# Kernel optimization log

Measured on AMD Instinct MI355X. Metric: run time of the kernel, lower is better.

Reference implementation:

```python
import jax, jax.numpy as jnp
import numpy as np

D_MODEL = 1024
N_HEADS = 16
HEAD_DIM = D_MODEL // N_HEADS


def setup_inputs() -> dict:
    key = jax.random.key(0)
    k1, k2, k3 = jax.random.split(key, 3)
    B, T = 4, 2048
    x = jax.random.normal(k1, (B, T, D_MODEL), dtype=jnp.float32)
    # torch Linear(d, 3d) weight is [3d, d]; y = x @ W^T. Store as [d, 3d] for x @ W.
    w_qkv = jax.random.normal(k2, (D_MODEL, 3 * D_MODEL), dtype=jnp.float32) * (D_MODEL ** -0.5)
    w_out = jax.random.normal(k3, (D_MODEL, D_MODEL), dtype=jnp.float32) * (D_MODEL ** -0.5)
    return {"x": x, "w_qkv": w_qkv, "w_out": w_out}


def reference(x, w_qkv, w_out):
    B, T, C = x.shape
    qkv = x @ w_qkv                             # [B, T, 3C]
    q, k, v = jnp.split(qkv, 3, axis=2)
    # [B, T, H, Dh] -> work in bthd layout via einsum
    q = q.reshape(B, T, N_HEADS, HEAD_DIM)
    k = k.reshape(B, T, N_HEADS, HEAD_DIM)
    v = v.reshape(B, T, N_HEADS, HEAD_DIM)
    scale = 1.0 / jnp.sqrt(jnp.asarray(HEAD_DIM, dtype=x.dtype))
    attn = jnp.einsum('bqhd,bkhd->bhqk', q, k) * scale   # [B, H, T, T]
    causal = jnp.tril(jnp.ones((T, T), dtype=bool))
    attn = jnp.where(causal, attn, jnp.asarray(-jnp.inf, dtype=attn.dtype))
    attn = jax.nn.softmax(attn, axis=-1)
    out = jnp.einsum('bhqk,bkhd->bqhd', attn, v).reshape(B, T, C)
    return out @ w_out
```

## Files before the change

kernel.cpp:

```cpp
#include <hip/hip_runtime.h>
#include <hip/hip_bf16.h>
#include <cstdint>


typedef __bf16 bf16x8 __attribute__((ext_vector_type(8)));
typedef __bf16 bf16x4 __attribute__((ext_vector_type(4)));
typedef float  f32x4  __attribute__((ext_vector_type(4)));
typedef float  f32x16 __attribute__((ext_vector_type(16)));
typedef unsigned int u32x4 __attribute__((ext_vector_type(4)));
typedef unsigned int u32x2 __attribute__((ext_vector_type(2)));

#define MFMA16(a, b, c) __builtin_amdgcn_mfma_f32_16x16x32_bf16((a), (b), (c), 0, 0, 0)
#define MFMA32(a, b, c) __builtin_amdgcn_mfma_f32_32x32x16_bf16((a), (b), (c), 0, 0, 0)

__device__ __forceinline__ float fexp2(float x) { return __builtin_amdgcn_exp2f(x); }

__device__ __forceinline__ void gload16(const void* g, void* lds) {
  __builtin_amdgcn_global_load_lds(
      (const __attribute__((address_space(1))) void*)(uintptr_t)g,
      (__attribute__((address_space(3))) void*)(uint32_t)(uintptr_t)lds,
      16, 0, 0);
}

__device__ __forceinline__ uint32_t cvtpk(float a, float b) {
  uint32_t r;
  asm("v_cvt_pk_bf16_f32 %0, %1, %2" : "=v"(r) : "v"(a), "v"(b));
  return r;
}

__device__ __forceinline__ float halfswap(float x, int hi) {
  uint32_t u = __builtin_bit_cast(uint32_t, x);
  u32x2 rr = __builtin_amdgcn_permlane32_swap(u, u, false, false);
  return __builtin_bit_cast(float, hi ? rr.x : rr.y);
}

__global__ __launch_bounds__(256) void k_f32_to_bf16(const float* __restrict__ in,
                                                     __bf16* __restrict__ out, int n) {
  int idx = (blockIdx.x * 256 + threadIdx.x) * 4;
  int stride = gridDim.x * 256 * 4;
  for (; idx < n; idx += stride) {
    float4 v = *(const float4*)(in + idx);
    bf16x4 o = { (__bf16)v.x, (__bf16)v.y, (__bf16)v.z, (__bf16)v.w };
    *(bf16x4*)(out + idx) = o;
  }
}

__global__ __launch_bounds__(256) void k_transpose_f32_bf16(const float* __restrict__ in,
                                                            __bf16* __restrict__ out,
                                                            int R, int C, float scale, int nscale) {
  __shared__ float t[64][65];
  const int r0 = blockIdx.y * 64, c0 = blockIdx.x * 64;
  const int tx = threadIdx.x & 15, ty = threadIdx.x >> 4;
#pragma unroll
  for (int rr = 0; rr < 4; ++rr) {
    int r = ty + rr * 16;
    float4 v = *(const float4*)(in + (size_t)(r0 + r) * C + c0 + tx * 4);
    t[r][tx * 4 + 0] = v.x; t[r][tx * 4 + 1] = v.y;
    t[r][tx * 4 + 2] = v.z; t[r][tx * 4 + 3] = v.w;
  }
  __syncthreads();
#pragma unroll
  for (int rr = 0; rr < 4; ++rr) {
    int c = ty + rr * 16;
    float sc = (c0 + c < nscale) ? scale : 1.0f;
    bf16x4 o = { (__bf16)(t[tx * 4 + 0][c] * sc), (__bf16)(t[tx * 4 + 1][c] * sc),
                 (__bf16)(t[tx * 4 + 2][c] * sc), (__bf16)(t[tx * 4 + 3][c] * sc) };
    *(bf16x4*)(out + (size_t)(c0 + c) * R + r0 + tx * 4) = o;
  }
}

template <typename OutT>
__global__ __launch_bounds__(256) void k_gemm_bt(const __bf16* __restrict__ A,
                                                 const __bf16* __restrict__ BT,
                                                 OutT* __restrict__ C,
                                                 int M, int N, int K) {
  __shared__ __align__(16) __bf16 At[128 * 32];
  __shared__ __align__(16) __bf16 Bt[128 * 32];
  const int tid = threadIdx.x;
  const int l = tid & 63, w = tid >> 6;
  const int wr = w >> 1, wc = w & 1;
  const int lr = l & 15, lk = l >> 4;
  const int bm0 = blockIdx.y * 128, bn0 = blockIdx.x * 128;

  const int sm = w * 16 + (l >> 2);
  const int sk = ((l & 3) ^ ((l >> 3) & 3)) * 8;
  const int xko = (lk ^ ((lr >> 1) & 3)) * 8;
  const __bf16* ga0 = A + (size_t)(bm0 + sm) * K + sk;
  const __bf16* ga1 = A + (size_t)(bm0 + 64 + sm) * K + sk;
  const __bf16* gb0 = BT + (size_t)(bn0 + sm) * K + sk;
  const __bf16* gb1 = BT + (size_t)(bn0 + 64 + sm) * K + sk;
  char* lA = (char*)At + w * 1024;
  char* lB = (char*)Bt + w * 1024;

  const f32x4 fz = {0.f, 0.f, 0.f, 0.f};
  f32x4 acc[4][4];
#pragma unroll
  for (int i = 0; i < 4; ++i) {
#pragma unroll
    for (int j = 0; j < 4; ++j) acc[i][j] = fz;
  }

  for (int k0 = 0; k0 < K; k0 += 32) {
    gload16(ga0, lA);
    gload16(ga1, lA + 4096);
    gload16(gb0, lB);
    gload16(gb1, lB + 4096);
    ga0 += 32; ga1 += 32; gb0 += 32; gb1 += 32;
    __syncthreads();
    bf16x8 af[4], bfr[4];
#pragma unroll
    for (int i = 0; i < 4; ++i)
      af[i] = *(const bf16x8*)(At + (wr * 64 + i * 16 + lr) * 32 + xko);
#pragma unroll
    for (int j = 0; j < 4; ++j)
      bfr[j] = *(const bf16x8*)(Bt + (wc * 64 + j * 16 + lr) * 32 + xko);
#pragma unroll
    for (int i = 0; i < 4; ++i) {
#pragma unroll
      for (int j = 0; j < 4; ++j) acc[i][j] = MFMA16(af[i], bfr[j], acc[i][j]);
    }
    __syncthreads();
  }

#pragma unroll
  for (int i = 0; i < 4; ++i) {
#pragma unroll
    for (int j = 0; j < 4; ++j) {
#pragma unroll
      for (int jj = 0; jj < 4; ++jj) {
        int row = bm0 + wr * 64 + i * 16 + lk * 4 + jj;
        int col = bn0 + wc * 64 + j * 16 + lr;
        C[(size_t)row * N + col] = (OutT)acc[i][j][jj];
      }
    }
  }
}

__global__ __launch_bounds__(512, 2) void k_gemm256(const __bf16* __restrict__ A,
                                                    const __bf16* __restrict__ BT,
                                                    __bf16* __restrict__ C,
                                                    __bf16* __restrict__ VT,
                                                    int M, int N, int K) {
  __shared__ __align__(16) __bf16 SMEM[4][2][128 * 64];
  __bf16 (*Als)[2][128 * 64] = &SMEM[0];
  __bf16 (*Bls)[2][128 * 64] = &SMEM[2];
  const int tid = threadIdx.x;
  const int l = tid & 63, w = tid >> 6;
  const int wm = w >> 2, wn = w & 3;
  const int wnh = wn >> 1, wnl = wn & 1;
  const int lr = l & 15, lk = l >> 4, lr7 = lr & 7;
  const int bm0 = blockIdx.y * 256, bn0 = blockIdx.x * 256;
  const int sr0 = w * 8 + (l >> 3);
  const int sc0 = ((l & 7) ^ (l >> 3)) * 8;
  const int xo0 = (lk ^ lr7) * 8;
  const int xo1 = ((4 + lk) ^ lr7) * 8;

#define STAGE_A(KT, H) do {                                                      \
    const __bf16* s_ = A + (size_t)(bm0 + (H) * 128 + sr0) * K + (KT) * 64 + sc0; \
    char* d_ = (char*)&Als[(KT) & 1][H][0] + w * 1024;                            \
    gload16(s_, d_);                                                              \
    gload16(s_ + (size_t)64 * K, d_ + 8192);                                      \
  } while (0)
#define STAGE_B(KT, H) do {                                                       \
    const __bf16* s_ = BT + (size_t)(bn0 + (H) * 128 + sr0) * K + (KT) * 64 + sc0; \
    char* d_ = (char*)&Bls[(KT) & 1][H][0] + w * 1024;                             \
    gload16(s_, d_);                                                               \
    gload16(s_ + (size_t)64 * K, d_ + 8192);                                       \
  } while (0)
#define LDA(SLOT, QM) do {                                                  \
    _Pragma("unroll") for (int f_ = 0; f_ < 4; ++f_) {                      \
      const __bf16* rp_ = &Als[SLOT][wm][0] + ((QM) * 64 + f_ * 16 + lr) * 64; \
      af[f_][0] = *(const bf16x8*)(rp_ + xo0);                              \
      af[f_][1] = *(const bf16x8*)(rp_ + xo1);                              \
    }                                                                       \
  } while (0)
#define LDB(SLOT, QN) do {                                                  \
    _Pragma("unroll") for (int g_ = 0; g_ < 2; ++g_) {                      \
      const __bf16* rp_ = &Bls[SLOT][wnh][0] + (wnl * 64 + (QN) * 32 + g_ * 16 + lr) * 64; \
      bq[QN][g_][0] = *(const bf16x8*)(rp_ + xo0);                          \
      bq[QN][g_][1] = *(const bf16x8*)(rp_ + xo1);                          \
    }                                                                       \
  } while (0)
#define MFMAQ(QM, QN) do {                                                  \
    __builtin_amdgcn_s_setprio(1);                                          \
    _Pragma("unroll") for (int f_ = 0; f_ < 4; ++f_) {                      \
      _Pragma("unroll") for (int g_ = 0; g_ < 2; ++g_) {                    \
        acc[(QM) * 4 + f_][(QN) * 2 + g_] =                                 \
            MFMA16(af[f_][0], bq[QN][g_][0], acc[(QM) * 4 + f_][(QN) * 2 + g_]); \
        acc[(QM) * 4 + f_][(QN) * 2 + g_] =                                 \
            MFMA16(af[f_][1], bq[QN][g_][1], acc[(QM) * 4 + f_][(QN) * 2 + g_]); \
      }                                                                     \
    }                                                                       \
    __builtin_amdgcn_s_setprio(0);                                          \
  } while (0)
#define BAR() asm volatile("s_barrier" ::: "memory")
#define VMCNT2() asm volatile("s_waitcnt vmcnt(2)" ::: "memory")
#define VMCNT0() asm volatile("s_waitcnt vmcnt(0)" ::: "memory")

  f32x4 acc[8][4];
  const f32x4 fz = {0.f, 0.f, 0.f, 0.f};
#pragma unroll
  for (int m = 0; m < 8; ++m) {
#pragma unroll
    for (int n = 0; n < 4; ++n) acc[m][n] = fz;
  }
  bf16x8 af[4][2], bq[2][2][2];

  STAGE_A(0, 0); STAGE_A(0, 1); STAGE_B(0, 0); STAGE_B(0, 1); STAGE_A(1, 0);
  VMCNT2();
  BAR();

  const int NT = K >> 7;
#pragma unroll 1
  for (int t = 0; t < NT; ++t) {
    const int k1 = 2 * t + 1, k2 = 2 * t + 2, k3 = 2 * t + 3;
    const bool last = (t == NT - 1);
    LDA(0, 0); LDB(0, 0);
    STAGE_A(k1, 1);
    BAR(); MFMAQ(0, 0); BAR();
    LDB(0, 1);
    STAGE_B(k1, 0);
    BAR(); MFMAQ(0, 1); BAR();
    LDA(0, 1);
    STAGE_B(k1, 1);
    BAR(); MFMAQ(1, 1); BAR();
    if (!last) { STAGE_A(k2, 0); VMCNT2(); } else { VMCNT0(); }
    BAR(); MFMAQ(1, 0); BAR();
    LDA(1, 0); LDB(1, 0);
    if (!last) STAGE_A(k2, 1);
    BAR(); MFMAQ(0, 0); BAR();
    LDB(1, 1);
    if (!last) STAGE_B(k2, 0);
    BAR(); MFMAQ(0, 1); BAR();
    LDA(1, 1);
    if (!last) STAGE_B(k2, 1);
    BAR(); MFMAQ(1, 1); BAR();
    if (!last) { STAGE_A(k3, 0); VMCNT2(); }
    BAR(); MFMAQ(1, 0); BAR();
  }

  if (VT != nullptr && bn0 >= 2048) {
    __bf16* tb = &SMEM[0][0][0];
    const int LDT = 264;
    const int bb = bm0 >> 11, tbase = bm0 & 2047;
#pragma unroll 1
    for (int hp = 0; hp < 2; ++hp) {
      if (wnh == hp) {
#pragma unroll
        for (int m = 0; m < 8; ++m) {
          const int tt = wm * 128 + (m >> 2) * 64 + (m & 3) * 16 + lk * 4;
#pragma unroll
          for (int n = 0; n < 4; ++n) {
            const int lcol = wnl * 64 + (n >> 1) * 32 + (n & 1) * 16 + lr;
            bf16x4 o = { (__bf16)acc[m][n][0], (__bf16)acc[m][n][1],
                         (__bf16)acc[m][n][2], (__bf16)acc[m][n][3] };
            *(bf16x4*)(tb + lcol * LDT + tt) = o;
          }
        }
      }
      __syncthreads();
#pragma unroll
      for (int it = 0; it < 8; ++it) {
        const int slot = it * 512 + tid;
        const int r = slot >> 5, toff = (slot & 31) * 8;
        bf16x8 v = *(const bf16x8*)(tb + r * LDT + toff);
        const int vcol = (bn0 - 2048) + hp * 128 + r;
        const int hc = vcol >> 6, d = vcol & 63;
        *(bf16x8*)(VT + ((size_t)((bb * 16 + hc) * 64 + d)) * 2048 + tbase + toff) = v;
      }
      if (hp == 0) __syncthreads();
    }
  } else {
#pragma unroll
    for (int m = 0; m < 8; ++m) {
      const int row = bm0 + wm * 128 + (m >> 2) * 64 + (m & 3) * 16 + lk * 4;
#pragma unroll
      for (int n = 0; n < 4; ++n) {
        const int col = bn0 + wn * 64 + (n >> 1) * 32 + (n & 1) * 16 + lr;
#pragma unroll
        for (int jj = 0; jj < 4; ++jj)
          C[(size_t)(row + jj) * N + col] = (__bf16)acc[m][n][jj];
      }
    }
  }
#undef STAGE_A
#undef STAGE_B
#undef LDA
#undef LDB
#undef MFMAQ
#undef BAR
#undef VMCNT2
#undef VMCNT0
}

__global__ __launch_bounds__(256, 2) void k_attn(const __bf16* __restrict__ qkv,
                                                 const __bf16* __restrict__ vt,
                                                 __bf16* __restrict__ ctx) {
  const int id = blockIdx.x;
  const int wg = (id & 7) * 64 + (id >> 3);
  const int p  = wg & 7;
  const int hb = wg >> 3;
  const int h = hb & 15, b = hb >> 4;

  const int l = threadIdx.x & 63, w = threadIdx.x >> 6;
  const int q = l & 31, hi = l >> 5, l7 = l & 7;

  __shared__ __align__(16) __bf16 KVs[3][2][64 * 64];

  const int srow = w * 8 + (l >> 3);
  const int scol = ((l & 7) ^ (l >> 3)) * 8;

  const __bf16* gK0 = qkv + (size_t)(b * 2048 + srow) * 3072 + 1024 + h * 64 + scol;
  const __bf16* gV0 = vt + ((size_t)((b * 16 + h) * 64 + srow)) * 2048 + scol;

  const float NEG = -1e30f;

  bf16x8 ones;
#pragma unroll
  for (int i = 0; i < 8; ++i) ones[i] = (__bf16)1.0f;

#define STG(BUF) do {                                                        \
    char* dK_ = (char*)&KVs[BUF][0][0] + w * 1024;                           \
    char* dV_ = (char*)&KVs[BUF][1][0] + w * 1024;                           \
    gload16(kp, dK_);                                                        \
    gload16(kp + (size_t)32 * 3072, dK_ + 4096);                             \
    gload16(vp, dV_);                                                        \
    gload16(vp + (size_t)32 * 2048, dV_ + 4096);                             \
    kp += (size_t)64 * 3072;                                                 \
    vp += 64;                                                                \
  } while (0)

#define ATTN_TILE(BUF, NXT) do {                                             \
    const int kv0 = kvt * 64;                                                \
    if (kvt + 1 < nkv) {                                                     \
      STG(NXT);                                                              \
      asm volatile("s_waitcnt vmcnt(4)" ::: "memory");                       \
    } else {                                                                 \
      asm volatile("s_waitcnt vmcnt(0)" ::: "memory");                       \
    }                                                                        \
    asm volatile("s_barrier" ::: "memory");                                  \
    if (kvt <= kvlast) {                                                     \
      const __bf16* Kb = &KVs[BUF][0][0];                                    \
      const __bf16* Vb = &KVs[BUF][1][0];                                    \
      f32x16 s0 = (f32x16)(0.0f), s1 = (f32x16)(0.0f);                       \
      __builtin_amdgcn_s_setprio(1);                                         \
      _Pragma("unroll") for (int d0 = 0; d0 < 4; ++d0) {                     \
        bf16x8 k0 = *(const bf16x8*)(Kb + (size_t)q * 64 + (((d0 * 2 + hi) ^ l7) * 8)); \
        bf16x8 k1 = *(const bf16x8*)(Kb + (size_t)(32 + q) * 64 + (((d0 * 2 + hi) ^ l7) * 8)); \
        s0 = MFMA32(k0, qf[d0], s0);                                         \
        s1 = MFMA32(k1, qf[d0], s1);                                         \
      }                                                                      \
      __builtin_amdgcn_s_setprio(0);                                         \
      if (kvt == kvlast) {                                                   \
        _Pragma("unroll") for (int r = 0; r < 16; ++r) {                     \
          const int kl = (r & 3) + 8 * (r >> 2) + 4 * hi;                    \
          if (kv0 + kl > qg) s0[r] = NEG;                                    \
          if (kv0 + 32 + kl > qg) s1[r] = NEG;                               \
        }                                                                    \
      }                                                                      \
      float t[8];                                                            \
      _Pragma("unroll") for (int i = 0; i < 8; ++i)                          \
        t[i] = fmaxf(fmaxf(s0[i], s0[i + 8]), fmaxf(s1[i], s1[i + 8]));      \
      _Pragma("unroll") for (int i = 0; i < 4; ++i) t[i] = fmaxf(t[i], t[i + 4]); \
      float mt = fmaxf(fmaxf(t[0], t[1]), fmaxf(t[2], t[3]));                \
      mt = fmaxf(mt, halfswap(mt, hi));                                      \
      if (!__all(mt - m_run <= 8.0f)) {                                      \
        const float al = fexp2(m_run - mt);                                  \
        _Pragma("unroll") for (int r = 0; r < 16; ++r) {                     \
          o0[r] *= al; o1[r] *= al; os[r] *= al;                             \
        }                                                                    \
        m_run = mt;                                                          \
      }                                                                      \
      _Pragma("unroll") for (int r = 0; r < 16; ++r) {                       \
        s0[r] = fexp2(s0[r] - m_run);                                        \
        s1[r] = fexp2(s1[r] - m_run);                                        \
      }                                                                      \
      uint32_t c0[8], c1[8];                                                 \
      _Pragma("unroll") for (int j = 0; j < 8; ++j) {                        \
        c0[j] = cvtpk(s0[2 * j], s0[2 * j + 1]);                             \
        c1[j] = cvtpk(s1[2 * j], s1[2 * j + 1]);                             \
      }                                                                      \
      u32x4 pk[4];                                                           \
      {                                                                      \
        u32x2 r0 = __builtin_amdgcn_permlane32_swap(c0[0], c0[2], false, false); \
        u32x2 r1 = __builtin_amdgcn_permlane32_swap(c0[1], c0[3], false, false); \
        u32x2 r2 = __builtin_amdgcn_permlane32_swap(c0[4], c0[6], false, false); \
        u32x2 r3 = __builtin_amdgcn_permlane32_swap(c0[5], c0[7], false, false); \
        pk[0].x = r0.x; pk[0].y = r1.x; pk[0].z = r0.y; pk[0].w = r1.y;      \
        pk[1].x = r2.x; pk[1].y = r3.x; pk[1].z = r2.y; pk[1].w = r3.y;      \
        u32x2 r4 = __builtin_amdgcn_permlane32_swap(c1[0], c1[2], false, false); \
        u32x2 r5 = __builtin_amdgcn_permlane32_swap(c1[1], c1[3], false, false); \
        u32x2 r6 = __builtin_amdgcn_permlane32_swap(c1[4], c1[6], false, false); \
        u32x2 r7 = __builtin_amdgcn_permlane32_swap(c1[5], c1[7], false, false); \
        pk[2].x = r4.x; pk[2].y = r5.x; pk[2].z = r4.y; pk[2].w = r5.y;      \
        pk[3].x = r6.x; pk[3].y = r7.x; pk[3].z = r6.y; pk[3].w = r7.y;      \
      }                                                                      \
      bf16x8 pf[4];                                                          \
      _Pragma("unroll") for (int kc = 0; kc < 4; ++kc)                       \
        pf[kc] = __builtin_bit_cast(bf16x8, pk[kc]);                         \
      __builtin_amdgcn_s_setprio(1);                                         \
      _Pragma("unroll") for (int kc = 0; kc < 4; ++kc) {                     \
        bf16x8 vf0 = *(const bf16x8*)(Vb + (size_t)q * 64 + (((kc * 2 + hi) ^ l7) * 8)); \
        o0 = MFMA32(vf0, pf[kc], o0);                                        \
      }                                                                      \
      _Pragma("unroll") for (int kc = 0; kc < 4; ++kc) {                     \
        bf16x8 vf1 = *(const bf16x8*)(Vb + (size_t)(32 + q) * 64 + (((kc * 2 + hi) ^ l7) * 8)); \
        o1 = MFMA32(vf1, pf[kc], o1);                                        \
      }                                                                      \
      _Pragma("unroll") for (int kc = 0; kc < 4; ++kc)                       \
        os = MFMA32(ones, pf[kc], os);         \
      __builtin_amdgcn_s_setprio(0);                                         \
    }                                                                        \
  } while (0)

#pragma unroll 1
  for (int ti = 0; ti < 2; ++ti) {
    const int qb = ti ? p : 15 - p;
    const int q0w = qb * 128 + w * 32;
    const int qg = q0w + q;
    const int nkv = 2 * qb + 2;
    const int kvlast = (q0w + 31) >> 6;

    const __bf16* qp = qkv + (size_t)(b * 2048 + qg) * 3072 + h * 64 + hi * 8;
    bf16x8 qf[4];
#pragma unroll
    for (int d0 = 0; d0 < 4; ++d0) qf[d0] = *(const bf16x8*)(qp + d0 * 16);

    float m_run = NEG;
    f32x16 o0 = (f32x16)(0.0f), o1 = (f32x16)(0.0f), os = (f32x16)(0.0f);

    const __bf16* kp = gK0;
    const __bf16* vp = gV0;

    STG(0);
    int kvt = 0;
    while (true) {
      ATTN_TILE(0, 1); if (++kvt == nkv) break;
      ATTN_TILE(1, 2); if (++kvt == nkv) break;
      ATTN_TILE(2, 0); if (++kvt == nkv) break;
    }
    __syncthreads();

    const float inv = 1.0f / os[0];
    __bf16* Ol = &KVs[0][0][0];
#pragma unroll
    for (int r = 0; r < 16; ++r) {
      const int d = (r & 3) + 8 * (r >> 2) + 4 * hi;
      Ol[(w * 32 + q) * 72 + d]      = (__bf16)(o0[r] * inv);
      Ol[(w * 32 + q) * 72 + 32 + d] = (__bf16)(o1[r] * inv);
    }
    __syncthreads();
    {
      const int row = threadIdx.x >> 1, half = threadIdx.x & 1;
      const __bf16* src = Ol + row * 72 + half * 32;
      __bf16* dst = ctx + (size_t)(b * 2048 + qb * 128 + row) * 1024 + h * 64 + half * 32;
#pragma unroll
      for (int i = 0; i < 4; ++i)
        *(bf16x8*)(dst + i * 8) = *(const bf16x8*)(src + i * 8);
    }
    __syncthreads();
  }
#undef STG
#undef ATTN_TILE
}

extern "C" void kernel_launch(void* const* d_in, const int* in_sizes, int n_in,
                              void* d_out, int out_size, void* d_ws, size_t ws_size,
                              hipStream_t stream) {
  const float* x    = (const float*)d_in[0];
  const float* wqkv = (const float*)d_in[1];
  const float* wout = (const float*)d_in[2];
  float* out = (float*)d_out;

  char* ws = (char*)d_ws;
  __bf16* xb    = (__bf16*)(ws);
  __bf16* wqkvT = (__bf16*)(ws + 16777216);
  __bf16* woutT = (__bf16*)(ws + 23068672);
  __bf16* qkvb  = (__bf16*)(ws + 25165824);
  __bf16* vtb   = (__bf16*)(ws + 75497472);
  __bf16* ctx   = (__bf16*)(ws + 92274688);

  const float qscale = 0.125f * 1.44269504088896340736f;

  k_f32_to_bf16<<<2048, 256, 0, stream>>>(x, xb, 8192 * 1024);
  k_transpose_f32_bf16<<<dim3(48, 16), 256, 0, stream>>>(wqkv, wqkvT, 1024, 3072, qscale, 1024);
  k_transpose_f32_bf16<<<dim3(16, 16), 256, 0, stream>>>(wout, woutT, 1024, 1024, 1.0f, 0);
  k_gemm256<<<dim3(12, 32), 512, 0, stream>>>(xb, wqkvT, qkvb, vtb, 8192, 3072, 1024);
  k_attn<<<512, 256, 0, stream>>>(qkvb, vtb, ctx);
  k_gemm_bt<float><<<dim3(8, 64), 256, 0, stream>>>(ctx, woutT, out, 8192, 1024, 1024);
}
```

Before: 167.5 us.

## Unify GEMMs into templated 128x256 pipelined kernel with XCD-aware block swizzle

Replaces the 256x256 QKV GEMM and the simple 128x128 output-projection GEMM with one templated 128x256-tile kernel. It keeps the double-buffered global-to-LDS pipeline and uses a swizzled block mapping that spreads consecutive tiles across the eight XCD groups. The QKV projection gets twice as many blocks, which should fill the GPU better. The output projection now gets the deeper pipelined schedule instead of a single-buffer loop. Smaller M tiles reduce per-block data reuse and change the V-transpose epilogue layout.

```diff
diff --git a/kernel.cpp b/kernel.cpp
--- a/kernel.cpp
+++ b/kernel.cpp
@@ -70,143 +70,82 @@
 }
 
 template <typename OutT>
-__global__ __launch_bounds__(256) void k_gemm_bt(const __bf16* __restrict__ A,
-                                                 const __bf16* __restrict__ BT,
-                                                 OutT* __restrict__ C,
-                                                 int M, int N, int K) {
-  __shared__ __align__(16) __bf16 At[128 * 32];
-  __shared__ __align__(16) __bf16 Bt[128 * 32];
-  const int tid = threadIdx.x;
-  const int l = tid & 63, w = tid >> 6;
-  const int wr = w >> 1, wc = w & 1;
-  const int lr = l & 15, lk = l >> 4;
-  const int bm0 = blockIdx.y * 128, bn0 = blockIdx.x * 128;
-
-  const int sm = w * 16 + (l >> 2);
-  const int sk = ((l & 3) ^ ((l >> 3) & 3)) * 8;
-  const int xko = (lk ^ ((lr >> 1) & 3)) * 8;
-  const __bf16* ga0 = A + (size_t)(bm0 + sm) * K + sk;
-  const __bf16* ga1 = A + (size_t)(bm0 + 64 + sm) * K + sk;
-  const __bf16* gb0 = BT + (size_t)(bn0 + sm) * K + sk;
-  const __bf16* gb1 = BT + (size_t)(bn0 + 64 + sm) * K + sk;
-  char* lA = (char*)At + w * 1024;
-  char* lB = (char*)Bt + w * 1024;
-
-  const f32x4 fz = {0.f, 0.f, 0.f, 0.f};
-  f32x4 acc[4][4];
-#pragma unroll
-  for (int i = 0; i < 4; ++i) {
-#pragma unroll
-    for (int j = 0; j < 4; ++j) acc[i][j] = fz;
-  }
-
-  for (int k0 = 0; k0 < K; k0 += 32) {
-    gload16(ga0, lA);
-    gload16(ga1, lA + 4096);
-    gload16(gb0, lB);
-    gload16(gb1, lB + 4096);
-    ga0 += 32; ga1 += 32; gb0 += 32; gb1 += 32;
-    __syncthreads();
-    bf16x8 af[4], bfr[4];
-#pragma unroll
-    for (int i = 0; i < 4; ++i)
-      af[i] = *(const bf16x8*)(At + (wr * 64 + i * 16 + lr) * 32 + xko);
-#pragma unroll
-    for (int j = 0; j < 4; ++j)
-      bfr[j] = *(const bf16x8*)(Bt + (wc * 64 + j * 16 + lr) * 32 + xko);
-#pragma unroll
-    for (int i = 0; i < 4; ++i) {
-#pragma unroll
-      for (int j = 0; j < 4; ++j) acc[i][j] = MFMA16(af[i], bfr[j], acc[i][j]);
-    }
-    __syncthreads();
-  }
-
-#pragma unroll
-  for (int i = 0; i < 4; ++i) {
-#pragma unroll
-    for (int j = 0; j < 4; ++j) {
-#pragma unroll
-      for (int jj = 0; jj < 4; ++jj) {
-        int row = bm0 + wr * 64 + i * 16 + lk * 4 + jj;
-        int col = bn0 + wc * 64 + j * 16 + lr;
-        C[(size_t)row * N + col] = (OutT)acc[i][j][jj];
-      }
-    }
-  }
-}
-
-__global__ __launch_bounds__(512, 2) void k_gemm256(const __bf16* __restrict__ A,
+__global__ __launch_bounds__(512, 2) void k_gemm128(const __bf16* __restrict__ A,
                                                     const __bf16* __restrict__ BT,
-                                                    __bf16* __restrict__ C,
+                                                    OutT* __restrict__ C,
                                                     __bf16* __restrict__ VT,
                                                     int M, int N, int K) {
-  __shared__ __align__(16) __bf16 SMEM[4][2][128 * 64];
-  __bf16 (*Als)[2][128 * 64] = &SMEM[0];
-  __bf16 (*Bls)[2][128 * 64] = &SMEM[2];
+  __shared__ __align__(16) __bf16 SMEM[6][128 * 64];
   const int tid = threadIdx.x;
   const int l = tid & 63, w = tid >> 6;
   const int wm = w >> 2, wn = w & 3;
   const int wnh = wn >> 1, wnl = wn & 1;
   const int lr = l & 15, lk = l >> 4, lr7 = lr & 7;
-  const int bm0 = blockIdx.y * 256, bn0 = blockIdx.x * 256;
+
+  const int lin = blockIdx.y * gridDim.x + blockIdx.x;
+  const int cpx = (gridDim.x * gridDim.y) >> 3;
+  const int swz = (lin & 7) * cpx + (lin >> 3);
+  const int bm0 = (swz / gridDim.x) * 128;
+  const int bn0 = (swz % gridDim.x) * 256;
+
   const int sr0 = w * 8 + (l >> 3);
   const int sc0 = ((l & 7) ^ (l >> 3)) * 8;
   const int xo0 = (lk ^ lr7) * 8;
   const int xo1 = ((4 + lk) ^ lr7) * 8;
 
-#define STAGE_A(KT, H) do {                                                      \
-    const __bf16* s_ = A + (size_t)(bm0 + (H) * 128 + sr0) * K + (KT) * 64 + sc0; \
-    char* d_ = (char*)&Als[(KT) & 1][H][0] + w * 1024;                            \
+#define STAGE_A(KT) do {                                                          \
+    const __bf16* s_ = A + (size_t)(bm0 + sr0) * K + (KT) * 64 + sc0;             \
+    char* d_ = (char*)&SMEM[(KT) & 1][0] + w * 1024;                              \
     gload16(s_, d_);                                                              \
     gload16(s_ + (size_t)64 * K, d_ + 8192);                                      \
   } while (0)
 #define STAGE_B(KT, H) do {                                                       \
     const __bf16* s_ = BT + (size_t)(bn0 + (H) * 128 + sr0) * K + (KT) * 64 + sc0; \
-    char* d_ = (char*)&Bls[(KT) & 1][H][0] + w * 1024;                             \
+    char* d_ = (char*)&SMEM[2 + ((KT) & 1) * 2 + (H)][0] + w * 1024;               \
     gload16(s_, d_);                                                               \
     gload16(s_ + (size_t)64 * K, d_ + 8192);                                       \
   } while (0)
-#define LDA(SLOT, QM) do {                                                  \
-    _Pragma("unroll") for (int f_ = 0; f_ < 4; ++f_) {                      \
-      const __bf16* rp_ = &Als[SLOT][wm][0] + ((QM) * 64 + f_ * 16 + lr) * 64; \
-      af[f_][0] = *(const bf16x8*)(rp_ + xo0);                              \
-      af[f_][1] = *(const bf16x8*)(rp_ + xo1);                              \
-    }                                                                       \
-  } while (0)
-#define LDB(SLOT, QN) do {                                                  \
-    _Pragma("unroll") for (int g_ = 0; g_ < 2; ++g_) {                      \
-      const __bf16* rp_ = &Bls[SLOT][wnh][0] + (wnl * 64 + (QN) * 32 + g_ * 16 + lr) * 64; \
-      bq[QN][g_][0] = *(const bf16x8*)(rp_ + xo0);                          \
-      bq[QN][g_][1] = *(const bf16x8*)(rp_ + xo1);                          \
-    }                                                                       \
-  } while (0)
-#define MFMAQ(QM, QN) do {                                                  \
-    __builtin_amdgcn_s_setprio(1);                                          \
-    _Pragma("unroll") for (int f_ = 0; f_ < 4; ++f_) {                      \
-      _Pragma("unroll") for (int g_ = 0; g_ < 2; ++g_) {                    \
-        acc[(QM) * 4 + f_][(QN) * 2 + g_] =                                 \
-            MFMA16(af[f_][0], bq[QN][g_][0], acc[(QM) * 4 + f_][(QN) * 2 + g_]); \
-        acc[(QM) * 4 + f_][(QN) * 2 + g_] =                                 \
-            MFMA16(af[f_][1], bq[QN][g_][1], acc[(QM) * 4 + f_][(QN) * 2 + g_]); \
-      }                                                                     \
-    }                                                                       \
-    __builtin_amdgcn_s_setprio(0);                                          \
+#define LDA(SLOT, QM) do {                                                        \
+    _Pragma("unroll") for (int f_ = 0; f_ < 2; ++f_) {                            \
+      const __bf16* rp_ = &SMEM[SLOT][0] + (wm * 64 + (QM) * 32 + f_ * 16 + lr) * 64; \
+      af[f_][0] = *(const bf16x8*)(rp_ + xo0);                                    \
+      af[f_][1] = *(const bf16x8*)(rp_ + xo1);                                    \
+    }                                                                             \
+  } while (0)
+#define LDB(SLOT, QN) do {                                                        \
+    _Pragma("unroll") for (int g_ = 0; g_ < 2; ++g_) {                            \
+      const __bf16* rp_ = &SMEM[2 + (SLOT) * 2 + wnh][0] +                        \
+                          (wnl * 64 + (QN) * 32 + g_ * 16 + lr) * 64;             \
+      bq[QN][g_][0] = *(const bf16x8*)(rp_ + xo0);                                \
+      bq[QN][g_][1] = *(const bf16x8*)(rp_ + xo1);                                \
+    }                                                                             \
+  } while (0)
+#define MFMAQ(QM, QN) do {                                                        \
+    __builtin_amdgcn_s_setprio(1);                                                \
+    _Pragma("unroll") for (int f_ = 0; f_ < 2; ++f_) {                            \
+      _Pragma("unroll") for (int g_ = 0; g_ < 2; ++g_) {                          \
+        acc[(QM) * 2 + f_][(QN) * 2 + g_] =                                       \
+            MFMA16(af[f_][0], bq[QN][g_][0], acc[(QM) * 2 + f_][(QN) * 2 + g_]);  \
+        acc[(QM) * 2 + f_][(QN) * 2 + g_] =                                       \
+            MFMA16(af[f_][1], bq[QN][g_][1], acc[(QM) * 2 + f_][(QN) * 2 + g_]);  \
+      }                                                                           \
+    }                                                                             \
+    __builtin_amdgcn_s_setprio(0);                                                \
   } while (0)
 #define BAR() asm volatile("s_barrier" ::: "memory")
 #define VMCNT2() asm volatile("s_waitcnt vmcnt(2)" ::: "memory")
 #define VMCNT0() asm volatile("s_waitcnt vmcnt(0)" ::: "memory")
 
-  f32x4 acc[8][4];
+  f32x4 acc[4][4];
   const f32x4 fz = {0.f, 0.f, 0.f, 0.f};
 #pragma unroll
-  for (int m = 0; m < 8; ++m) {
+  for (int m = 0; m < 4; ++m) {
 #pragma unroll
     for (int n = 0; n < 4; ++n) acc[m][n] = fz;
   }
-  bf16x8 af[4][2], bq[2][2][2];
-
-  STAGE_A(0, 0); STAGE_A(0, 1); STAGE_B(0, 0); STAGE_B(0, 1); STAGE_A(1, 0);
+  bf16x8 af[2][2], bq[2][2][2];
+
+  STAGE_A(0); STAGE_B(0, 0); STAGE_B(0, 1); STAGE_A(1);
   VMCNT2();
   BAR();
 
@@ -216,70 +155,62 @@
     const int k1 = 2 * t + 1, k2 = 2 * t + 2, k3 = 2 * t + 3;
     const bool last = (t == NT - 1);
     LDA(0, 0); LDB(0, 0);
-    STAGE_A(k1, 1);
+    STAGE_B(k1, 0);
     BAR(); MFMAQ(0, 0); BAR();
     LDB(0, 1);
-    STAGE_B(k1, 0);
+    STAGE_B(k1, 1);
     BAR(); MFMAQ(0, 1); BAR();
     LDA(0, 1);
-    STAGE_B(k1, 1);
     BAR(); MFMAQ(1, 1); BAR();
-    if (!last) { STAGE_A(k2, 0); VMCNT2(); } else { VMCNT0(); }
+    if (!last) { STAGE_A(k2); VMCNT2(); } else { VMCNT0(); }
     BAR(); MFMAQ(1, 0); BAR();
     LDA(1, 0); LDB(1, 0);
-    if (!last) STAGE_A(k2, 1);
+    if (!last) STAGE_B(k2, 0);
     BAR(); MFMAQ(0, 0); BAR();
     LDB(1, 1);
-    if (!last) STAGE_B(k2, 0);
+    if (!last) STAGE_B(k2, 1);
     BAR(); MFMAQ(0, 1); BAR();
     LDA(1, 1);
-    if (!last) STAGE_B(k2, 1);
     BAR(); MFMAQ(1, 1); BAR();
-    if (!last) { STAGE_A(k3, 0); VMCNT2(); }
+    if (!last) { STAGE_A(k3); VMCNT2(); }
     BAR(); MFMAQ(1, 0); BAR();
   }
 
   if (VT != nullptr && bn0 >= 2048) {
-    __bf16* tb = &SMEM[0][0][0];
-    const int LDT = 264;
+    __bf16* tb = &SMEM[0][0];
+    const int LDT = 136;
     const int bb = bm0 >> 11, tbase = bm0 & 2047;
-#pragma unroll 1
-    for (int hp = 0; hp < 2; ++hp) {
-      if (wnh == hp) {
-#pragma unroll
-        for (int m = 0; m < 8; ++m) {
-          const int tt = wm * 128 + (m >> 2) * 64 + (m & 3) * 16 + lk * 4;
-#pragma unroll
-          for (int n = 0; n < 4; ++n) {
-            const int lcol = wnl * 64 + (n >> 1) * 32 + (n & 1) * 16 + lr;
-            bf16x4 o = { (__bf16)acc[m][n][0], (__bf16)acc[m][n][1],
-                         (__bf16)acc[m][n][2], (__bf16)acc[m][n][3] };
-            *(bf16x4*)(tb + lcol * LDT + tt) = o;
-          }
-        }
+#pragma unroll
+    for (int m = 0; m < 4; ++m) {
+      const int tt = wm * 64 + m * 16 + lk * 4;
+#pragma unroll
+      for (int n = 0; n < 4; ++n) {
+        const int lcol = wn * 64 + (n >> 1) * 32 + (n & 1) * 16 + lr;
+        bf16x4 o = { (__bf16)acc[m][n][0], (__bf16)acc[m][n][1],
+                     (__bf16)acc[m][n][2], (__bf16)acc[m][n][3] };
+        *(bf16x4*)(tb + lcol * LDT + tt) = o;
       }
-      __syncthreads();
-#pragma unroll
-      for (int it = 0; it < 8; ++it) {
-        const int slot = it * 512 + tid;
-        const int r = slot >> 5, toff = (slot & 31) * 8;
-        bf16x8 v = *(const bf16x8*)(tb + r * LDT + toff);
-        const int vcol = (bn0 - 2048) + hp * 128 + r;
-        const int hc = vcol >> 6, d = vcol & 63;
-        *(bf16x8*)(VT + ((size_t)((bb * 16 + hc) * 64 + d)) * 2048 + tbase + toff) = v;
-      }
-      if (hp == 0) __syncthreads();
+    }
+    __syncthreads();
+#pragma unroll
+    for (int it = 0; it < 8; ++it) {
+      const int slot = it * 512 + tid;
+      const int r = slot >> 4, toff = (slot & 15) * 8;
+      bf16x8 v = *(const bf16x8*)(tb + r * LDT + toff);
+      const int vcol = (bn0 - 2048) + r;
+      const int hc = vcol >> 6, d = vcol & 63;
+      *(bf16x8*)(VT + ((size_t)((bb * 16 + hc) * 64 + d)) * 2048 + tbase + toff) = v;
     }
   } else {
 #pragma unroll
-    for (int m = 0; m < 8; ++m) {
-      const int row = bm0 + wm * 128 + (m >> 2) * 64 + (m & 3) * 16 + lk * 4;
+    for (int m = 0; m < 4; ++m) {
+      const int row = bm0 + wm * 64 + m * 16 + lk * 4;
 #pragma unroll
       for (int n = 0; n < 4; ++n) {
         const int col = bn0 + wn * 64 + (n >> 1) * 32 + (n & 1) * 16 + lr;
 #pragma unroll
         for (int jj = 0; jj < 4; ++jj)
-          C[(size_t)(row + jj) * N + col] = (__bf16)acc[m][n][jj];
+          C[(size_t)(row + jj) * N + col] = (OutT)acc[m][n][jj];
       }
     }
   }
@@ -485,7 +416,7 @@
   k_f32_to_bf16<<<2048, 256, 0, stream>>>(x, xb, 8192 * 1024);
   k_transpose_f32_bf16<<<dim3(48, 16), 256, 0, stream>>>(wqkv, wqkvT, 1024, 3072, qscale, 1024);
   k_transpose_f32_bf16<<<dim3(16, 16), 256, 0, stream>>>(wout, woutT, 1024, 1024, 1.0f, 0);
-  k_gemm256<<<dim3(12, 32), 512, 0, stream>>>(xb, wqkvT, qkvb, vtb, 8192, 3072, 1024);
+  k_gemm128<__bf16><<<dim3(12, 64), 512, 0, stream>>>(xb, wqkvT, qkvb, vtb, 8192, 3072, 1024);
   k_attn<<<512, 256, 0, stream>>>(qkvb, vtb, ctx);
-  k_gemm_bt<float><<<dim3(8, 64), 256, 0, stream>>>(ctx, woutT, out, 8192, 1024, 1024);
-}
+  k_gemm128<float><<<dim3(4, 64), 512, 0, stream>>>(ctx, woutT, out, nullptr, 8192, 1024, 1024);
+}
```

Measured after the change: 157.7 us. 1.06x faster.
